# Kernel tuning notes

Hardware: AMD Instinct MI355X
Metric: run time of the kernel (lower is better)

Reference implementation:

```python
import jax, jax.numpy as jnp
import numpy as np

B, L, D, H = 4, 2048, 1024, 16
DH = D // H

def setup_inputs() -> dict:
    key = jax.random.key(0)
    k1, k2, k3 = jax.random.split(key, 3)
    x = jax.random.normal(k1, (B, L, D), dtype=jnp.float32)
    w_qkv = jax.random.normal(k2, (3 * D, D), dtype=jnp.float32) * (1.0 / np.sqrt(D))
    w_proj = jax.random.normal(k3, (D, D), dtype=jnp.float32) * (1.0 / np.sqrt(D))
    return {"x": x, "w_qkv": w_qkv, "w_proj": w_proj}

def reference(x, w_qkv, w_proj):
    b, l, d = x.shape
    scale = 1.0 / np.sqrt(DH)
    qkv = (x @ w_qkv.T).reshape(b, l, 3, H, DH)
    qkv = jnp.transpose(qkv, (2, 0, 3, 1, 4))
    q, k, v = qkv[0], qkv[1], qkv[2]
    scores = jnp.einsum('bhqd,bhkd->bhqk', q, k) * scale
    attn = jax.nn.softmax(scores, axis=-1)
    out = jnp.einsum('bhqk,bhkd->bhqd', attn, v)
    out = jnp.transpose(out, (0, 2, 1, 3)).reshape(b, l, d)
    return out @ w_proj.T
```

## Files before the change

### kernel.cpp

```cpp
#include <hip/hip_runtime.h>
#include <hip/hip_bf16.h>


typedef __bf16  bf16x8  __attribute__((ext_vector_type(8)));
typedef float   floatx4 __attribute__((ext_vector_type(4)));

__device__ __forceinline__ void async_ld16(const void* g, void* lds_base_uniform) {
  __builtin_amdgcn_global_load_lds(
      (const __attribute__((address_space(1))) void*)g,
      (__attribute__((address_space(3))) void*)lds_base_uniform,
      16, 0, 0);
}

__device__ __forceinline__ int detect_bf16(const void* p) {
  const unsigned short* u = (const unsigned short*)p;
  int sane = 0;
#pragma unroll 4
  for (int i = 0; i < 64; ++i) {
    unsigned short w = u[2 * i];
    int e = (w >> 7) & 0xFF;
    sane += (w == 0 || (e >= 100 && e <= 150)) ? 1 : 0;
  }
  return sane >= 32;
}

__device__ __forceinline__ bf16x8 ld8_f32cvt(const void* base, size_t elem) {
  const float* p = (const float*)base + elem;
  floatx4 u0 = *(const floatx4*)p;
  floatx4 u1 = *(const floatx4*)(p + 4);
  bf16x8 v;
  v[0] = (__bf16)u0[0]; v[1] = (__bf16)u0[1]; v[2] = (__bf16)u0[2]; v[3] = (__bf16)u0[3];
  v[4] = (__bf16)u1[0]; v[5] = (__bf16)u1[1]; v[6] = (__bf16)u1[2]; v[7] = (__bf16)u1[3];
  return v;
}

template<int CTRL>
__device__ __forceinline__ float dpp_f(float x) {
  return __builtin_bit_cast(float,
      __builtin_amdgcn_update_dpp(0, __builtin_bit_cast(int, x), CTRL, 0xF, 0xF, true));
}
__device__ __forceinline__ float row16_sum(float x) {
  x += dpp_f<0xB1>(x);
  x += dpp_f<0x4E>(x);
  x += dpp_f<0x141>(x);
  x += dpp_f<0x140>(x);
  return x;
}

__launch_bounds__(256)
__global__ void cvt3_kernel(const void* __restrict__ s0, __bf16* __restrict__ d0, int n0,
                            const void* __restrict__ s1, __bf16* __restrict__ d1, int n1,
                            const void* __restrict__ s2, __bf16* __restrict__ d2) {
  int u = blockIdx.x * blockDim.x + threadIdx.x;
  const void* src; __bf16* dst;
  if (u < n0)           { src = s0; dst = d0; }
  else if (u < n0 + n1) { src = s1; dst = d1; u -= n0; }
  else                  { src = s2; dst = d2; u -= n0 + n1; }
  const int is_bf16 = detect_bf16(src);
  const size_t e = (size_t)u * 8;
  if (is_bf16) *(bf16x8*)(dst + e) = *(const bf16x8*)((const __bf16*)src + e);
  else         *(bf16x8*)(dst + e) = ld8_f32cvt(src, e);
}

template<int EPI>
__launch_bounds__(256, 2)
__global__ void gemm_bt_kernel(const __bf16* __restrict__ A,
                               const __bf16* __restrict__ B,
                               const void* __restrict__ oprobe,
                               void* __restrict__ Cout,
                               __bf16* __restrict__ qb,
                               __bf16* __restrict__ kb,
                               __bf16* __restrict__ vtb,
                               int M, int N, int K)
{
  __shared__ __align__(16) __bf16 As[128 * 32];
  __shared__ __align__(16) __bf16 Bs[128 * 32];

  const int flat = blockIdx.x;
  const int m0 = (((flat & 7) << 3) | ((flat >> 3) & 7)) << 7;
  const int n0 = (flat >> 6) << 7;

  const int tid  = threadIdx.x;
  const int wave = tid >> 6;
  const int lane = tid & 63;
  const int quad = lane >> 4;
  const int l16  = lane & 15;
  const int wm   = wave >> 1;
  const int wn   = wave & 1;

  const int r_in   = lane >> 2;
  const int cchunk = lane & 3;

  const __bf16* Ab = A + (size_t)m0 * K;
  const __bf16* Bb = B + (size_t)n0 * K;

  floatx4 acc[4][4];
#pragma unroll
  for (int i = 0; i < 4; ++i)
#pragma unroll
    for (int j = 0; j < 4; ++j)
      acc[i][j] = (floatx4){0.f, 0.f, 0.f, 0.f};

  const int ca0 = wave * 2;
  for (int k0 = 0; k0 < K; k0 += 32) {
#pragma unroll
    for (int i = 0; i < 2; ++i) {
      const int ca  = ca0 + i;
      const int row = ca * 16 + r_in;
      async_ld16(Ab + (size_t)row * K + k0 + cchunk * 8, (char*)As + ca * 1024);
      async_ld16(Bb + (size_t)row * K + k0 + cchunk * 8, (char*)Bs + ca * 1024);
    }
    __syncthreads();

    bf16x8 af[4], bfr[4];
#pragma unroll
    for (int tt = 0; tt < 4; ++tt) {
      af[tt]  = *(const bf16x8*)&As[(wm * 64 + tt * 16 + l16) * 32 + quad * 8];
      bfr[tt] = *(const bf16x8*)&Bs[(wn * 64 + tt * 16 + l16) * 32 + quad * 8];
    }
#pragma unroll
    for (int mt = 0; mt < 4; ++mt)
#pragma unroll
      for (int nt = 0; nt < 4; ++nt)
        acc[mt][nt] = __builtin_amdgcn_mfma_f32_16x16x32_bf16(af[mt], bfr[nt], acc[mt][nt], 0, 0, 0);
    __syncthreads();
  }

  const int out_bf16 = (EPI == 1) ? detect_bf16(oprobe) : 0;

#pragma unroll
  for (int mt = 0; mt < 4; ++mt) {
#pragma unroll
    for (int nt = 0; nt < 4; ++nt) {
      const int n_idx = n0 + wn * 64 + nt * 16 + l16;
      const int mbase = m0 + wm * 64 + mt * 16 + quad * 4;
      if (EPI == 1) {
        if (out_bf16) {
#pragma unroll
          for (int r = 0; r < 4; ++r)
            ((__bf16*)Cout)[(size_t)(mbase + r) * N + n_idx] = (__bf16)acc[mt][nt][r];
        } else {
#pragma unroll
          for (int r = 0; r < 4; ++r)
            ((float*)Cout)[(size_t)(mbase + r) * N + n_idx] = acc[mt][nt][r];
        }
      } else {
        const int sel = n_idx >> 10;
        const int rem = n_idx & 1023;
        const int h   = rem >> 6;
        const int dh  = rem & 63;
#pragma unroll
        for (int r = 0; r < 4; ++r) {
          const int m_idx = mbase + r;
          const int b  = m_idx >> 11;
          const int l  = m_idx & 2047;
          const int bh = b * 16 + h;
          const __bf16 v = (__bf16)acc[mt][nt][r];
          if (sel == 0)      qb [((size_t)bh * 2048 + l) * 64 + dh] = v;
          else if (sel == 1) kb [((size_t)bh * 2048 + l) * 64 + dh] = v;
          else               vtb[((size_t)bh * 64 + dh) * 2048 + l] = v;
        }
      }
    }
  }
}

__launch_bounds__(256, 4)
__global__ void attn_kernel(const __bf16* __restrict__ qb,
                            const __bf16* __restrict__ kb,
                            const __bf16* __restrict__ vtb,
                            __bf16* __restrict__ ob )
{
  __shared__ __align__(16) __bf16 Ks[64 * 72];
  __shared__ __align__(16) __bf16 Vs[80 * 72];
  __shared__ __align__(16) __bf16 Ps[4][32 * 72];

  const int tid  = threadIdx.x;
  const int wave = tid >> 6;
  const int lane = tid & 63;
  const int quad = lane >> 4;
  const int l16  = lane & 15;

  const int bh = blockIdx.y;
  const int q0 = blockIdx.x * 128;

  const __bf16* Qp = qb  + (size_t)bh * 2048 * 64;
  const __bf16* Kp = kb  + (size_t)bh * 2048 * 64;
  const __bf16* Vp = vtb + (size_t)bh * 64 * 2048;

  for (int i = tid; i < 16 * 72; i += 256)
    Vs[64 * 72 + i] = (i < 72) ? (__bf16)1.0f : (__bf16)0.0f;
  __syncthreads();

  const float C1 = 0.125f * 1.44269504f;
  const float C2 = -8.0f  * 1.44269504f;

  bf16x8 aq[2][2];
#pragma unroll
  for (int rt = 0; rt < 2; ++rt) {
    const __bf16* qrow = Qp + (size_t)(q0 + wave * 32 + rt * 16 + l16) * 64;
    aq[rt][0] = *(const bf16x8*)(qrow + quad * 8);
    aq[rt][1] = *(const bf16x8*)(qrow + 32 + quad * 8);
  }

  floatx4 o[2][4], o5[2];
#pragma unroll
  for (int rt = 0; rt < 2; ++rt) {
    o5[rt] = (floatx4){0.f, 0.f, 0.f, 0.f};
#pragma unroll
    for (int dt = 0; dt < 4; ++dt) o[rt][dt] = (floatx4){0.f, 0.f, 0.f, 0.f};
  }

  for (int kt = 0; kt < 32; ++kt) {
    const int k0 = kt * 64;
#pragma unroll
    for (int it = 0; it < 2; ++it) {
      const int c   = tid + it * 256;
      const int row = c >> 3;
      const int cc  = c & 7;
      *(bf16x8*)&Ks[row * 72 + cc * 8] =
          *(const bf16x8*)(Kp + (size_t)(k0 + row) * 64 + cc * 8);
      *(bf16x8*)&Vs[row * 72 + cc * 8] =
          *(const bf16x8*)(Vp + (size_t)row * 2048 + k0 + cc * 8);
    }
    __syncthreads();

    floatx4 s[2][4];
#pragma unroll
    for (int nt = 0; nt < 4; ++nt) {
      const int krow = nt * 16 + l16;
      bf16x8 bk0 = *(const bf16x8*)&Ks[krow * 72 + quad * 8];
      bf16x8 bk1 = *(const bf16x8*)&Ks[krow * 72 + 32 + quad * 8];
#pragma unroll
      for (int rt = 0; rt < 2; ++rt) {
        floatx4 z = (floatx4){0.f, 0.f, 0.f, 0.f};
        z = __builtin_amdgcn_mfma_f32_16x16x32_bf16(aq[rt][0], bk0, z, 0, 0, 0);
        z = __builtin_amdgcn_mfma_f32_16x16x32_bf16(aq[rt][1], bk1, z, 0, 0, 0);
        s[rt][nt] = z;
      }
    }

#pragma unroll
    for (int rt = 0; rt < 2; ++rt) {
      __bf16* Pw = &Ps[wave][0];
#pragma unroll
      for (int nt = 0; nt < 4; ++nt)
#pragma unroll
        for (int r = 0; r < 4; ++r) {
          const float p = __builtin_amdgcn_exp2f(fmaf(s[rt][nt][r], C1, C2));
          Pw[(rt * 16 + quad * 4 + r) * 72 + nt * 16 + l16] = (__bf16)p;
        }
    }

    __builtin_amdgcn_wave_barrier();

    bf16x8 ap[2][2];
#pragma unroll
    for (int rt = 0; rt < 2; ++rt) {
      ap[rt][0] = *(const bf16x8*)&Ps[wave][(rt * 16 + l16) * 72 + quad * 8];
      ap[rt][1] = *(const bf16x8*)&Ps[wave][(rt * 16 + l16) * 72 + 32 + quad * 8];
    }

#pragma unroll
    for (int dt = 0; dt < 4; ++dt) {
      const int vrow = dt * 16 + l16;
      bf16x8 bv0 = *(const bf16x8*)&Vs[vrow * 72 + quad * 8];
      bf16x8 bv1 = *(const bf16x8*)&Vs[vrow * 72 + 32 + quad * 8];
#pragma unroll
      for (int rt = 0; rt < 2; ++rt) {
        o[rt][dt] = __builtin_amdgcn_mfma_f32_16x16x32_bf16(ap[rt][0], bv0, o[rt][dt], 0, 0, 0);
        o[rt][dt] = __builtin_amdgcn_mfma_f32_16x16x32_bf16(ap[rt][1], bv1, o[rt][dt], 0, 0, 0);
      }
    }
    {
      const int vrow = 64 + l16;
      bf16x8 bv0 = *(const bf16x8*)&Vs[vrow * 72 + quad * 8];
      bf16x8 bv1 = *(const bf16x8*)&Vs[vrow * 72 + 32 + quad * 8];
#pragma unroll
      for (int rt = 0; rt < 2; ++rt) {
        o5[rt] = __builtin_amdgcn_mfma_f32_16x16x32_bf16(ap[rt][0], bv0, o5[rt], 0, 0, 0);
        o5[rt] = __builtin_amdgcn_mfma_f32_16x16x32_bf16(ap[rt][1], bv1, o5[rt], 0, 0, 0);
      }
    }
    __syncthreads();
  }

  const int b = bh >> 4;
  const int h = bh & 15;
#pragma unroll
  for (int rt = 0; rt < 2; ++rt)
#pragma unroll
    for (int r = 0; r < 4; ++r) {
      const float lv  = row16_sum(l16 == 0 ? o5[rt][r] : 0.f);
      const float inv = 1.f / lv;
      const size_t rowbase =
          ((size_t)b * 2048 + q0 + wave * 32 + rt * 16 + quad * 4 + r) * 1024 + h * 64;
#pragma unroll
      for (int dt = 0; dt < 4; ++dt)
        ob[rowbase + dt * 16 + l16] = (__bf16)(o[rt][dt][r] * inv);
    }
}

extern "C" void kernel_launch(void* const* d_in, const int* in_sizes, int n_in,
                              void* d_out, int out_size, void* d_ws, size_t ws_size,
                              hipStream_t stream)
{
  (void)in_sizes; (void)n_in; (void)out_size; (void)ws_size;

  const void* x     = d_in[0];
  const void* wqkv  = d_in[1];
  const void* wproj = d_in[2];

  const size_t NX    = (size_t)8192 * 1024;
  const size_t NWQKV = (size_t)3072 * 1024;
  const size_t NWPRJ = (size_t)1024 * 1024;

  __bf16* qbuf   = (__bf16*)d_ws;
  __bf16* kbuf   = qbuf + NX;
  __bf16* vtbuf  = kbuf + NX;
  __bf16* abuf   = vtbuf + NX;
  __bf16* xb     = abuf + NX;
  __bf16* wqkvb  = xb + NX;
  __bf16* wprojb = wqkvb + NWQKV;

  dim3 blk(256);

  cvt3_kernel<<<dim3((NX + NWQKV + NWPRJ) / 2048), blk, 0, stream>>>(
      x, xb, NX / 8, wqkv, wqkvb, NWQKV / 8, wproj, wprojb);

  gemm_bt_kernel<0><<<dim3(24 * 64), blk, 0, stream>>>(
      xb, wqkvb, nullptr, nullptr, qbuf, kbuf, vtbuf, 8192, 3072, 1024);

  attn_kernel<<<dim3(2048 / 128, 64), blk, 0, stream>>>(qbuf, kbuf, vtbuf, abuf);

  gemm_bt_kernel<1><<<dim3(8 * 64), blk, 0, stream>>>(
      abuf, wprojb, wproj, d_out, nullptr, nullptr, nullptr, 8192, 1024, 1024);
}
```

Baseline: 329.0 us.

## Prefetch next K/V tile into registers and vectorize P and V stores

The attention loop now loads the next K/V tile from global memory into registers while the current tile is being computed, then writes it to LDS between two barriers, so load latency overlaps with MFMA work. The S computation swaps its MFMA operands to produce S transposed, which lets each lane write four packed P values as one bf16x4 LDS store instead of scalar stores. The QKV epilogue writes V-transposed as packed bf16x4 vectors and simplifies the Q/K index math. The prefetch costs extra registers and one more barrier per iteration, which could reduce occupancy.

```diff
diff --git a/kernel.cpp b/kernel.cpp
--- a/kernel.cpp
+++ b/kernel.cpp
@@ -3,6 +3,7 @@
 
 
 typedef __bf16  bf16x8  __attribute__((ext_vector_type(8)));
+typedef __bf16  bf16x4  __attribute__((ext_vector_type(4)));
 typedef float   floatx4 __attribute__((ext_vector_type(4)));
 
 __device__ __forceinline__ void async_ld16(const void* g, void* lds_base_uniform) {
@@ -149,16 +150,19 @@
         const int rem = n_idx & 1023;
         const int h   = rem >> 6;
         const int dh  = rem & 63;
-#pragma unroll
-        for (int r = 0; r < 4; ++r) {
-          const int m_idx = mbase + r;
-          const int b  = m_idx >> 11;
-          const int l  = m_idx & 2047;
-          const int bh = b * 16 + h;
-          const __bf16 v = (__bf16)acc[mt][nt][r];
-          if (sel == 0)      qb [((size_t)bh * 2048 + l) * 64 + dh] = v;
-          else if (sel == 1) kb [((size_t)bh * 2048 + l) * 64 + dh] = v;
-          else               vtb[((size_t)bh * 64 + dh) * 2048 + l] = v;
+        const int b   = mbase >> 11;
+        const int l   = mbase & 2047;
+        const int bh  = b * 16 + h;
+        if (sel == 2) {
+          bf16x4 pk;
+#pragma unroll
+          for (int r = 0; r < 4; ++r) pk[r] = (__bf16)acc[mt][nt][r];
+          *(bf16x4*)&vtb[((size_t)bh * 64 + dh) * 2048 + l] = pk;
+        } else {
+          __bf16* dstb = (sel == 0 ? qb : kb) + ((size_t)bh * 2048 + l) * 64 + dh;
+#pragma unroll
+          for (int r = 0; r < 4; ++r)
+            dstb[(size_t)r * 64] = (__bf16)acc[mt][nt][r];
         }
       }
     }
@@ -190,7 +194,6 @@
 
   for (int i = tid; i < 16 * 72; i += 256)
     Vs[64 * 72 + i] = (i < 72) ? (__bf16)1.0f : (__bf16)0.0f;
-  __syncthreads();
 
   const float C1 = 0.125f * 1.44269504f;
   const float C2 = -8.0f  * 1.44269504f;
@@ -211,45 +214,54 @@
     for (int dt = 0; dt < 4; ++dt) o[rt][dt] = (floatx4){0.f, 0.f, 0.f, 0.f};
   }
 
+  const int srow0 = tid >> 3;
+  const int scc   = (tid & 7) * 8;
+
+  {
+#pragma unroll
+    for (int it = 0; it < 2; ++it) {
+      const int row = srow0 + it * 32;
+      *(bf16x8*)&Ks[row * 72 + scc] = *(const bf16x8*)(Kp + (size_t)row * 64 + scc);
+      *(bf16x8*)&Vs[row * 72 + scc] = *(const bf16x8*)(Vp + (size_t)row * 2048 + scc);
+    }
+  }
+  __syncthreads();
+
   for (int kt = 0; kt < 32; ++kt) {
-    const int k0 = kt * 64;
+    const int kn = (((kt + 1) & 31) << 6);
+    bf16x8 kreg[2], vreg[2];
 #pragma unroll
     for (int it = 0; it < 2; ++it) {
-      const int c   = tid + it * 256;
-      const int row = c >> 3;
-      const int cc  = c & 7;
-      *(bf16x8*)&Ks[row * 72 + cc * 8] =
-          *(const bf16x8*)(Kp + (size_t)(k0 + row) * 64 + cc * 8);
-      *(bf16x8*)&Vs[row * 72 + cc * 8] =
-          *(const bf16x8*)(Vp + (size_t)row * 2048 + k0 + cc * 8);
-    }
-    __syncthreads();
-
-    floatx4 s[2][4];
+      const int row = srow0 + it * 32;
+      kreg[it] = *(const bf16x8*)(Kp + (size_t)(kn + row) * 64 + scc);
+      vreg[it] = *(const bf16x8*)(Vp + (size_t)row * 2048 + kn + scc);
+    }
+
+    floatx4 st[2][4];
 #pragma unroll
     for (int nt = 0; nt < 4; ++nt) {
       const int krow = nt * 16 + l16;
-      bf16x8 bk0 = *(const bf16x8*)&Ks[krow * 72 + quad * 8];
-      bf16x8 bk1 = *(const bf16x8*)&Ks[krow * 72 + 32 + quad * 8];
+      bf16x8 ak0 = *(const bf16x8*)&Ks[krow * 72 + quad * 8];
+      bf16x8 ak1 = *(const bf16x8*)&Ks[krow * 72 + 32 + quad * 8];
 #pragma unroll
       for (int rt = 0; rt < 2; ++rt) {
         floatx4 z = (floatx4){0.f, 0.f, 0.f, 0.f};
-        z = __builtin_amdgcn_mfma_f32_16x16x32_bf16(aq[rt][0], bk0, z, 0, 0, 0);
-        z = __builtin_amdgcn_mfma_f32_16x16x32_bf16(aq[rt][1], bk1, z, 0, 0, 0);
-        s[rt][nt] = z;
+        z = __builtin_amdgcn_mfma_f32_16x16x32_bf16(ak0, aq[rt][0], z, 0, 0, 0);
+        z = __builtin_amdgcn_mfma_f32_16x16x32_bf16(ak1, aq[rt][1], z, 0, 0, 0);
+        st[rt][nt] = z;
       }
     }
 
 #pragma unroll
     for (int rt = 0; rt < 2; ++rt) {
-      __bf16* Pw = &Ps[wave][0];
-#pragma unroll
-      for (int nt = 0; nt < 4; ++nt)
-#pragma unroll
-        for (int r = 0; r < 4; ++r) {
-          const float p = __builtin_amdgcn_exp2f(fmaf(s[rt][nt][r], C1, C2));
-          Pw[(rt * 16 + quad * 4 + r) * 72 + nt * 16 + l16] = (__bf16)p;
-        }
+#pragma unroll
+      for (int nt = 0; nt < 4; ++nt) {
+        bf16x4 pk;
+#pragma unroll
+        for (int r = 0; r < 4; ++r)
+          pk[r] = (__bf16)__builtin_amdgcn_exp2f(fmaf(st[rt][nt][r], C1, C2));
+        *(bf16x4*)&Ps[wave][(rt * 16 + l16) * 72 + nt * 16 + quad * 4] = pk;
+      }
     }
 
     __builtin_amdgcn_wave_barrier();
@@ -281,6 +293,14 @@
         o5[rt] = __builtin_amdgcn_mfma_f32_16x16x32_bf16(ap[rt][0], bv0, o5[rt], 0, 0, 0);
         o5[rt] = __builtin_amdgcn_mfma_f32_16x16x32_bf16(ap[rt][1], bv1, o5[rt], 0, 0, 0);
       }
+    }
+
+    __syncthreads();
+#pragma unroll
+    for (int it = 0; it < 2; ++it) {
+      const int row = srow0 + it * 32;
+      *(bf16x8*)&Ks[row * 72 + scc] = kreg[it];
+      *(bf16x8*)&Vs[row * 72 + scc] = vreg[it];
     }
     __syncthreads();
   }
```

Result: faster. 288.7 us (-12.3%).
